# Kernel optimization log

Measured on AMD Instinct MI355X. Metric: run time of the kernel, lower is better.

## Reference

```python
import jax, jax.numpy as jnp
import numpy as np

NUM_HEADS = 16
HEAD_DIM = 128
EMBED_DIM = 2048
BASE = 10000.0


def rope(x, offset=0):
    # x: [b, h, n, d]  rotary positional embedding (lrpe_type=1)
    d = x.shape[-1]
    n = x.shape[-2]
    inv_freq = 1.0 / (BASE ** (jnp.arange(0, d, 2, dtype=jnp.float32) / d))  # [d/2]
    pos = jnp.arange(n, dtype=jnp.float32) + offset                          # [n]
    ang = pos[:, None] * inv_freq[None, :]                                   # [n, d/2]
    cos, sin = jnp.cos(ang), jnp.sin(ang)
    x1, x2 = x[..., 0::2], x[..., 1::2]
    out1 = x1 * cos - x2 * sin
    out2 = x1 * sin + x2 * cos
    return jnp.stack([out1, out2], axis=-1).reshape(x.shape)


def setup_inputs() -> dict:
    key = jax.random.key(0)
    ks = jax.random.split(key, 5)
    b, n = 2, 2048
    std = 0.02
    x = jax.random.normal(ks[0], (b, n, EMBED_DIM), dtype=jnp.float32)
    Wq = jax.random.normal(ks[1], (NUM_HEADS * HEAD_DIM, EMBED_DIM), dtype=jnp.float32) * std
    Wkv = jax.random.normal(ks[2], (2 * HEAD_DIM, EMBED_DIM), dtype=jnp.float32) * std
    Wkvh = jax.random.normal(ks[3], (2 * NUM_HEADS, EMBED_DIM), dtype=jnp.float32) * std
    Wo = jax.random.normal(ks[4], (EMBED_DIM, NUM_HEADS * HEAD_DIM), dtype=jnp.float32) * std
    return {"x": x, "Wq": Wq, "Wkv": Wkv, "Wkvh": Wkvh, "Wo": Wo}


def reference(x, Wq, Wkv, Wkvh, Wo):
    b, n, _ = x.shape
    h, d = NUM_HEADS, HEAD_DIM
    q = x @ Wq.T                     # [b, n, h*d]
    kv = x @ Wkv.T                   # [b, n, 2d]
    kvh = x @ Wkvh.T                 # [b, n, 2h]  (mpa_activation='none')
    k, v = kv[..., :d], kv[..., d:]
    k_head, v_head = kvh[..., :h], kvh[..., h:]
    # gate_type=0: per-token outer product broadcast of the single kv to all heads
    k = jnp.einsum('bnd,bnh->bhnd', k, k_head)
    v = jnp.einsum('bnd,bnh->bhnd', v, v_head)
    q = q.reshape(b, n, h, d).transpose(0, 2, 1, 3)  # [b, h, n, d]
    q = rope(q)
    k = rope(k)
    scale = 1.0 / jnp.sqrt(jnp.float32(d))
    scores = jnp.einsum('bhqd,bhkd->bhqk', q, k) * scale
    causal = jnp.tril(jnp.ones((n, n), dtype=bool))
    scores = jnp.where(causal, scores, -jnp.inf)
    attn = jax.nn.softmax(scores, axis=-1)
    o = jnp.einsum('bhqk,bhkd->bhqd', attn, v)
    o = o.transpose(0, 2, 1, 3).reshape(b, n, h * d)
    return o @ Wo.T
```

## Files before the change

### kernel.cpp

```cpp
#include <hip/hip_runtime.h>
#include <stdint.h>

#define BB 2
#define HH 16
#define NN 2048
#define DD 128
#define EE 2048

typedef short s16x8 __attribute__((ext_vector_type(8)));
typedef float fx4 __attribute__((ext_vector_type(4)));

static __device__ __forceinline__ unsigned short f2bf(float f) {
  unsigned u = __builtin_bit_cast(unsigned, f);
  u += 0x7fffu + ((u >> 16) & 1u);
  return (unsigned short)(u >> 16);
}
static __device__ __forceinline__ float bf2f(unsigned short h) {
  unsigned u = ((unsigned)h) << 16;
  return __builtin_bit_cast(float, u);
}
static __device__ __forceinline__ void gload_lds16(const void* g, void* l) {
  __builtin_amdgcn_global_load_lds(
      (const __attribute__((address_space(1))) unsigned int*)g,
      (__attribute__((address_space(3))) unsigned int*)l, 16, 0, 0);
}
static __device__ __forceinline__ unsigned cvt_pk_bf16(float lo, float hi) {
  unsigned w;
  asm("v_cvt_pk_bf16_f32 %0, %1, %2" : "=v"(w) : "v"(lo), "v"(hi));
  return w;
}

__global__ __launch_bounds__(256) void f2b_all(const float* __restrict__ x,
                                               const float* __restrict__ Wq,
                                               const float* __restrict__ Wkv,
                                               const float* __restrict__ Wo,
                                               const float* __restrict__ Wkvh,
                                               unsigned short* __restrict__ xb,
                                               unsigned short* __restrict__ wqkv,
                                               unsigned short* __restrict__ wob,
                                               unsigned short* __restrict__ wkvhb) {
  int bid = blockIdx.x;
  const float* in;
  unsigned short* out;
  int i;
  if (bid < 8192) { in = x; out = xb; i = bid * 256 + threadIdx.x; }
  else if (bid < 12288) { in = Wq; out = wqkv; i = (bid - 8192) * 256 + threadIdx.x; }
  else if (bid < 12800) { in = Wkv; out = wqkv + 4194304; i = (bid - 12288) * 256 + threadIdx.x; }
  else if (bid < 16896) { in = Wo; out = wob; i = (bid - 12800) * 256 + threadIdx.x; }
  else { in = Wkvh; out = wkvhb; i = (bid - 16896) * 256 + threadIdx.x; }
  float4 v = ((const float4*)in)[i];
  uint2 o;
  o.x = ((unsigned)f2bf(v.y) << 16) | f2bf(v.x);
  o.y = ((unsigned)f2bf(v.w) << 16) | f2bf(v.z);
  ((uint2*)out)[i] = o;
}

#define GBK 64

#define GEMM_STAGE(LDSB, SRCBASE, rowb)                                        \
  _Pragma("unroll") for (int t = 0; t < 4; ++t) {                              \
    int r = wave * 32 + t * 8 + (lane >> 3);                                   \
    int ch = (lane & 7) ^ (r & 7);                                             \
    const unsigned char* src = (SRCBASE) + (size_t)r * (rowb) + ch * 16;       \
    gload_lds16(src, (void*)((LDSB) + (wave * 32 + t * 8) * 128));             \
  }

#define GEMM_LOOP_BODY                                                         \
  for (int k0 = 0; k0 < K; k0 += GBK) {                                        \
    const unsigned char* ag = Ag + (size_t)k0 * 2;                             \
    const unsigned char* bg = Bg + (size_t)k0 * 2;                             \
    __syncthreads();                                                           \
    GEMM_STAGE(Alds, ag, rowb)                                                 \
    GEMM_STAGE(Blds, bg, rowb)                                                 \
    __syncthreads();                                                           \
    _Pragma("unroll") for (int kk = 0; kk < 2; ++kk) {                         \
      s16x8 af[4], bf[4];                                                      \
      _Pragma("unroll") for (int i = 0; i < 4; ++i) {                          \
        int row = wr * 64 + i * 16 + lr;                                       \
        int chunk = (kk * 4 + g) ^ (row & 7);                                  \
        af[i] = *(const s16x8*)(Alds + row * 128 + chunk * 16);                \
      }                                                                        \
      _Pragma("unroll") for (int j = 0; j < 4; ++j) {                          \
        int row = wc * 64 + j * 16 + lr;                                       \
        int chunk = (kk * 4 + g) ^ (row & 7);                                  \
        bf[j] = *(const s16x8*)(Blds + row * 128 + chunk * 16);                \
      }                                                                        \
      _Pragma("unroll") for (int i = 0; i < 4; ++i)                            \
        _Pragma("unroll") for (int j = 0; j < 4; ++j)                          \
          acc[i][j] = __builtin_amdgcn_mfma_f32_16x16x32_bf16(af[i], bf[j],    \
                                                              acc[i][j], 0, 0, 0); \
    }                                                                          \
  }

#define GEMM_PROLOG                                                            \
  __shared__ alignas(16) unsigned char Alds[128 * 128];                        \
  __shared__ alignas(16) unsigned char Blds[128 * 128];                        \
  const int tid = threadIdx.x;                                                 \
  const int wave = tid >> 6, lane = tid & 63;                                  \
  const int g = lane >> 4, lr = lane & 15;                                     \
  const int mtiles = M / 128;                                                  \
  const int mt = blockIdx.x % mtiles, nt = blockIdx.x / mtiles;                \
  const int m0 = mt * 128, n0 = nt * 128;                                      \
  const int wr = wave >> 1, wc = wave & 1;                                     \
  fx4 acc[4][4];                                                               \
  _Pragma("unroll") for (int i = 0; i < 4; ++i)                                \
    _Pragma("unroll") for (int j = 0; j < 4; ++j)                              \
      acc[i][j] = (fx4){0.f, 0.f, 0.f, 0.f};                                   \
  const unsigned char* Ag = (const unsigned char*)(A + (size_t)m0 * K);        \
  const unsigned char* Bg = (const unsigned char*)(B + (size_t)n0 * K);        \
  const size_t rowb = (size_t)K * 2;

__global__ __launch_bounds__(256) void gemm_out(const unsigned short* __restrict__ A,
                                                const unsigned short* __restrict__ B,
                                                float* __restrict__ Cf,
                                                int M, int N, int K) {
  GEMM_PROLOG
  GEMM_LOOP_BODY
#pragma unroll
  for (int i = 0; i < 4; ++i) {
    int row = m0 + wr * 64 + i * 16 + 4 * g;
#pragma unroll
    for (int j = 0; j < 4; ++j) {
      int col = n0 + wc * 64 + j * 16 + lr;
#pragma unroll
      for (int r = 0; r < 4; ++r)
        Cf[(size_t)(row + r) * N + col] = acc[i][j][r];
    }
  }
}

__global__ __launch_bounds__(256) void gemm_qkv(const unsigned short* __restrict__ A,
                                                const unsigned short* __restrict__ B,
                                                unsigned short* __restrict__ qrope,
                                                unsigned short* __restrict__ kvb,
                                                int M, int N, int K) {
  GEMM_PROLOG
  GEMM_LOOP_BODY
#pragma unroll
  for (int j = 0; j < 4; ++j) {
    int col = n0 + wc * 64 + j * 16 + lr;
    if (col < 2048) {
      int hh = col >> 7, d = col & 127;
      float invf = __expf(-0.14391156831212787f * (float)(d >> 1));
      int par = d & 1;
#pragma unroll
      for (int i = 0; i < 4; ++i) {
#pragma unroll
        for (int r = 0; r < 4; ++r) {
          int row = m0 + wr * 64 + i * 16 + 4 * g + r;
          int n = row & (NN - 1), bq = row >> 11;
          float self = acc[i][j][r];
          float other = __shfl_xor(self, 1);
          float sn, cs;
          __sincosf((float)n * invf, &sn, &cs);
          float a = self * cs, bt = other * sn;
          float o = par ? (a + bt) : (a - bt);
          qrope[((size_t)(bq * HH + hh) * NN + n) * DD + d] = f2bf(o);
        }
      }
    } else {
      int c2 = col - 2048;
#pragma unroll
      for (int i = 0; i < 4; ++i) {
#pragma unroll
        for (int r = 0; r < 4; ++r) {
          int row = m0 + wr * 64 + i * 16 + 4 * g + r;
          kvb[(size_t)row * 256 + c2] = f2bf(acc[i][j][r]);
        }
      }
    }
  }
}

__global__ __launch_bounds__(256) void kvh_mfma(const unsigned short* __restrict__ X,
                                                const unsigned short* __restrict__ Wb,
                                                float* __restrict__ out) {
  const int tid = threadIdx.x;
  const int wave = tid >> 6, lane = tid & 63;
  const int g = lane >> 4, lr = lane & 15;
  const int rowbase = blockIdx.x * 32 + (wave & 1) * 16;
  const int colbase = (wave >> 1) * 16;

  const unsigned short* xr = X + (size_t)(rowbase + lr) * EE + 8 * g;
  const unsigned short* wr = Wb + (size_t)(colbase + lr) * EE + 8 * g;

  fx4 acc = (fx4){0.f, 0.f, 0.f, 0.f};
#pragma unroll 8
  for (int k0 = 0; k0 < EE; k0 += 32) {
    s16x8 a = *(const s16x8*)(xr + k0);
    s16x8 b = *(const s16x8*)(wr + k0);
    acc = __builtin_amdgcn_mfma_f32_16x16x32_bf16(a, b, acc, 0, 0, 0);
  }
  const int j = colbase + lr;
  const int head = j & 15, sel = j >> 4;
#pragma unroll
  for (int r = 0; r < 4; ++r) {
    int m = rowbase + 4 * g + r;
    int b = m >> 11, n = m & (NN - 1);
    out[(((size_t)(b * HH + head)) * NN + n) * 2 + sel] = acc[r];
  }
}

__global__ __launch_bounds__(256) void rope_k(const unsigned short* __restrict__ kv,
                                              unsigned short* __restrict__ ko) {
  int idx = blockIdx.x * 256 + threadIdx.x;
  int i = idx & 63;
  int bn = idx >> 6;
  int n = bn & (NN - 1);
  unsigned v = *(const unsigned*)(kv + (size_t)bn * 256 + 2 * i);
  float x1 = bf2f((unsigned short)(v & 0xffff));
  float x2 = bf2f((unsigned short)(v >> 16));
  float inv = __expf(-0.14391156831212787f * (float)i);
  float ang = (float)n * inv;
  float sn, cs;
  __sincosf(ang, &sn, &cs);
  float o1 = x1 * cs - x2 * sn, o2 = x1 * sn + x2 * cs;
  unsigned ov = ((unsigned)f2bf(o2) << 16) | f2bf(o1);
  *(unsigned*)(ko + (size_t)bn * DD + 2 * i) = ov;
}

__global__ __launch_bounds__(256) void vtrans(const unsigned short* __restrict__ kv,
                                              unsigned short* __restrict__ vT) {
  __shared__ unsigned short t[64][40];
  int bx = blockIdx.x;
  int b = bx >> 7;
  int d0 = ((bx >> 5) & 3) * 32;
  int n0 = (bx & 31) * 64;
  int tid = threadIdx.x;
  {
    int i = tid >> 2;
    int c = (tid & 3) * 8;
    s16x8 v = *(const s16x8*)(kv + ((size_t)(b * NN + n0 + i)) * 256 + 128 + d0 + c);
#pragma unroll
    for (int u = 0; u < 8; ++u) t[i][c + u] = (unsigned short)v[u];
  }
  __syncthreads();
  {
    int j = tid >> 3;
    int cc = (tid & 7) * 8;
    s16x8 o;
#pragma unroll
    for (int u = 0; u < 8; ++u) o[u] = (short)t[cc + u][j];
    *(s16x8*)(vT + ((size_t)(b * DD + d0 + j)) * NN + n0 + cc) = o;
  }
}

#define QB 128
#define KB 64

__global__ __launch_bounds__(512, 2) void attn(const unsigned short* __restrict__ Q,
                                               const unsigned short* __restrict__ Kr,
                                               const unsigned short* __restrict__ VT,
                                               const float* __restrict__ KVHP,
                                               unsigned short* __restrict__ O) {
  __shared__ alignas(16) unsigned char Klds[2 * 64 * 256];
  __shared__ alignas(16) unsigned char Vlds[2 * 128 * 128];
  __shared__ alignas(16) unsigned char Plds[16 * 16 * 128];
  __shared__ float2 mlbuf[4][2][16];

  const int qp = blockIdx.x;
  const int h = blockIdx.y;
  const int b = blockIdx.z;
  const int tid = threadIdx.x;
  const int wave = tid >> 6, lane = tid & 63;
  const int parity = wave >> 2, wq = wave & 3;
  const int g = lane >> 4, lr = lane & 15;
  const size_t bh = (size_t)(b * HH + h);

  const float scale2 = 0.08838834764831845f * 1.4426950408889634f;
  const unsigned short* Kb = Kr + (size_t)b * NN * DD;
  const unsigned short* VTb = VT + (size_t)b * DD * NN;
  const float2* KVp = (const float2*)KVHP + (size_t)(b * HH + h) * NN;

  unsigned char* Kl = Klds + parity * (64 * 256);
  unsigned char* Vl = Vlds + parity * (128 * 128);
  float* Obuf = (float*)Plds;

  auto STAGE = [&](int key0s) {
#pragma unroll
    for (int j = 0; j < 4; ++j) {
      int rl = wq * 16 + j * 4 + (lane >> 4);
      int ch = (lane & 15) ^ (rl & 7);
      const unsigned char* gp = (const unsigned char*)(Kb + (size_t)(key0s + rl) * DD) + ch * 16;
      gload_lds16(gp, (void*)(Kl + (wq * 16 + j * 4) * 256));
    }
#pragma unroll
    for (int j = 0; j < 4; ++j) {
      int row = wq * 32 + j * 8 + (lane >> 3);
      int c = lane & 7;
      const unsigned short* gp = VTb + (size_t)row * NN + key0s + ((c ^ (row & 7)) * 8);
      gload_lds16(gp, (void*)(Vl + (wq * 32 + j * 8) * 128));
    }
  };

  auto PHASE = [&](int qt) {
    const int qbase_w = qt * QB + wq * 32;

    s16x8 qf[2][4];
#pragma unroll
    for (int qq = 0; qq < 2; ++qq) {
      const unsigned short* qptr = Q + (bh * NN + qbase_w + qq * 16 + lr) * DD + 8 * g;
#pragma unroll
      for (int dc = 0; dc < 4; ++dc) qf[qq][dc] = *(const s16x8*)(qptr + dc * 32);
    }

    float m_run[2] = {-1e30f, -1e30f}, l_run[2] = {0.f, 0.f};
    fx4 oacc[2][8];
#pragma unroll
    for (int qq = 0; qq < 2; ++qq)
#pragma unroll
      for (int d = 0; d < 8; ++d) oacc[qq][d] = (fx4){0.f, 0.f, 0.f, 0.f};

    const int cnt = qt + 1;
    for (int i = 0; i < cnt; ++i) {
      const int key0 = (2 * i + parity) * KB;
      __syncthreads();
      fx4 khv[4], vhv[4];
#pragma unroll
      for (int kb = 0; kb < 4; ++kb) {
        const float4* kp = (const float4*)(KVp + key0 + kb * 16 + 4 * g);
        float4 f0 = kp[0];
        float4 f1 = kp[1];
        khv[kb] = (fx4){f0.x * scale2, f0.z * scale2, f1.x * scale2, f1.z * scale2};
        vhv[kb] = (fx4){f0.y, f0.w, f1.y, f1.w};
      }
      STAGE(key0);
      __syncthreads();

      if (key0 <= qbase_w + 31) {
        fx4 sacc[2][4];
#pragma unroll
        for (int qq = 0; qq < 2; ++qq)
#pragma unroll
          for (int kb = 0; kb < 4; ++kb) sacc[qq][kb] = (fx4){0.f, 0.f, 0.f, 0.f};
        __builtin_amdgcn_s_setprio(1);
#pragma unroll
        for (int kb = 0; kb < 4; ++kb) {
#pragma unroll
          for (int dc = 0; dc < 4; ++dc) {
            int key = kb * 16 + lr;
            int chunk = (dc * 4 + g) ^ (key & 7);
            s16x8 kf = *(const s16x8*)(Kl + key * 256 + chunk * 16);
            sacc[0][kb] = __builtin_amdgcn_mfma_f32_16x16x32_bf16(kf, qf[0][dc], sacc[0][kb], 0, 0, 0);
            sacc[1][kb] = __builtin_amdgcn_mfma_f32_16x16x32_bf16(kf, qf[1][dc], sacc[1][kb], 0, 0, 0);
          }
        }
        __builtin_amdgcn_s_setprio(0);

#pragma unroll
        for (int qq = 0; qq < 2; ++qq) {
          const int qg = qbase_w + qq * 16 + lr;
          float smax = -1e30f;
          if (key0 + 63 > qbase_w + qq * 16) {
#pragma unroll
            for (int kb = 0; kb < 4; ++kb) {
#pragma unroll
              for (int r = 0; r < 4; ++r) {
                int keyg = key0 + kb * 16 + 4 * g + r;
                float s = sacc[qq][kb][r] * khv[kb][r];
                if (keyg > qg) s = -1e30f;
                sacc[qq][kb][r] = s;
                smax = fmaxf(smax, s);
              }
            }
          } else {
#pragma unroll
            for (int kb = 0; kb < 4; ++kb) {
#pragma unroll
              for (int r = 0; r < 4; ++r) {
                float s = sacc[qq][kb][r] * khv[kb][r];
                sacc[qq][kb][r] = s;
                smax = fmaxf(smax, s);
              }
            }
          }
          smax = fmaxf(smax, __shfl_xor(smax, 16));
          smax = fmaxf(smax, __shfl_xor(smax, 32));
          if (!__all(smax - m_run[qq] <= 8.0f)) {
            float mnew = fmaxf(m_run[qq], smax);
            float corr = exp2f(m_run[qq] - mnew);
            m_run[qq] = mnew;
            l_run[qq] *= corr;
            float cr[4];
#pragma unroll
            for (int r = 0; r < 4; ++r) cr[r] = __shfl(corr, 4 * g + r);
#pragma unroll
            for (int d = 0; d < 8; ++d)
#pragma unroll
              for (int r = 0; r < 4; ++r) oacc[qq][d][r] *= cr[r];
          }
          float rsum = 0.f;
#pragma unroll
          for (int kb = 0; kb < 4; ++kb) {
            float p0 = exp2f(sacc[qq][kb][0] - m_run[qq]);
            float p1 = exp2f(sacc[qq][kb][1] - m_run[qq]);
            float p2 = exp2f(sacc[qq][kb][2] - m_run[qq]);
            float p3 = exp2f(sacc[qq][kb][3] - m_run[qq]);
            rsum += (p0 + p1) + (p2 + p3);
            uint2 w;
            w.x = cvt_pk_bf16(p0 * vhv[kb][0], p1 * vhv[kb][1]);
            w.y = cvt_pk_bf16(p2 * vhv[kb][2], p3 * vhv[kb][3]);
            int chunk = (kb * 2 + (g >> 1)) ^ (lr & 7);
            *(uint2*)(Plds + (wave * 2 + qq) * 2048 + lr * 128 + chunk * 16 + (g & 1) * 8) = w;
          }
          rsum += __shfl_xor(rsum, 16);
          rsum += __shfl_xor(rsum, 32);
          l_run[qq] += rsum;
        }

        s16x8 pa[2][2];
#pragma unroll
        for (int qq = 0; qq < 2; ++qq)
#pragma unroll
          for (int kk = 0; kk < 2; ++kk) {
            int chunk = (kk * 4 + g) ^ (lr & 7);
            pa[qq][kk] = *(const s16x8*)(Plds + (wave * 2 + qq) * 2048 + lr * 128 + chunk * 16);
          }
        __builtin_amdgcn_s_setprio(1);
#pragma unroll
        for (int dc = 0; dc < 8; ++dc) {
#pragma unroll
          for (int kk = 0; kk < 2; ++kk) {
            int d = dc * 16 + lr;
            int chunk = (kk * 4 + g) ^ (d & 7);
            s16x8 vf = *(const s16x8*)(Vl + d * 128 + chunk * 16);
            oacc[0][dc] = __builtin_amdgcn_mfma_f32_16x16x32_bf16(pa[0][kk], vf, oacc[0][dc], 0, 0, 0);
            oacc[1][dc] = __builtin_amdgcn_mfma_f32_16x16x32_bf16(pa[1][kk], vf, oacc[1][dc], 0, 0, 0);
          }
        }
        __builtin_amdgcn_s_setprio(0);
      }
    }

    __syncthreads();
    if (parity == 1 && g == 0) {
#pragma unroll
      for (int qq = 0; qq < 2; ++qq)
        mlbuf[wq][qq][lr] = make_float2(m_run[qq], l_run[qq]);
    }
    __syncthreads();
    float lC[2], af0[2][4], af1[2][4];
    if (parity == 0) {
#pragma unroll
      for (int qq = 0; qq < 2; ++qq) {
        float2 ml1 = mlbuf[wq][qq][lr];
        float M = fmaxf(m_run[qq], ml1.x);
        float a0 = exp2f(m_run[qq] - M);
        float a1 = exp2f(ml1.x - M);
        lC[qq] = l_run[qq] * a0 + ml1.y * a1;
#pragma unroll
        for (int r = 0; r < 4; ++r) {
          af0[qq][r] = __shfl(a0, 4 * g + r);
          af1[qq][r] = __shfl(a1, 4 * g + r);
        }
      }
    }
#pragma unroll
    for (int dh = 0; dh < 2; ++dh) {
      if (parity == 1) {
#pragma unroll
        for (int qq = 0; qq < 2; ++qq)
#pragma unroll
          for (int dc2 = 0; dc2 < 4; ++dc2)
#pragma unroll
            for (int r = 0; r < 4; ++r)
              Obuf[wq * 2048 + (qq * 16 + 4 * g + r) * 64 + dc2 * 16 + lr] =
                  oacc[qq][dh * 4 + dc2][r];
      }
      __syncthreads();
      if (parity == 0) {
#pragma unroll
        for (int qq = 0; qq < 2; ++qq)
#pragma unroll
          for (int dc2 = 0; dc2 < 4; ++dc2)
#pragma unroll
            for (int r = 0; r < 4; ++r) {
              float o1 = Obuf[wq * 2048 + (qq * 16 + 4 * g + r) * 64 + dc2 * 16 + lr];
              oacc[qq][dh * 4 + dc2][r] =
                  oacc[qq][dh * 4 + dc2][r] * af0[qq][r] + o1 * af1[qq][r];
            }
      }
      __syncthreads();
    }
    if (parity == 0) {
#pragma unroll
      for (int qq = 0; qq < 2; ++qq) {
        float inv = 1.0f / lC[qq];
#pragma unroll
        for (int r = 0; r < 4; ++r) {
          float invr = __shfl(inv, 4 * g + r);
          int qout = qbase_w + qq * 16 + 4 * g + r;
          unsigned short* orow = O + (((size_t)b * NN + qout) * HH + h) * DD;
#pragma unroll
          for (int dc = 0; dc < 8; ++dc) orow[dc * 16 + lr] = f2bf(oacc[qq][dc][r] * invr);
        }
      }
    }
  };

  PHASE(qp);
  PHASE(15 - qp);
}

extern "C" void kernel_launch(void* const* d_in, const int* in_sizes, int n_in,
                              void* d_out, int out_size, void* d_ws, size_t ws_size,
                              hipStream_t stream) {
  const float* x = (const float*)d_in[0];
  const float* Wq = (const float*)d_in[1];
  const float* Wkv = (const float*)d_in[2];
  const float* Wkvh = (const float*)d_in[3];
  const float* Wo = (const float*)d_in[4];
  float* out = (float*)d_out;
  char* ws = (char*)d_ws;

  unsigned short* xb    = (unsigned short*)(ws + 0);
  unsigned short* obuf  = xb;
  unsigned short* wqkv  = (unsigned short*)(ws + 16777216);
  unsigned short* wob   = (unsigned short*)(ws + 26214400);
  unsigned short* kvb   = (unsigned short*)(ws + 34603008);
  unsigned short* vtb   = (unsigned short*)(ws + 36700160);
  unsigned short* wkvhb = (unsigned short*)(ws + 53477376);
  float*          kvhb  = (float*)(ws + 53608448);
  unsigned short* qrope = (unsigned short*)(ws + 54132736);
  unsigned short* krope = (unsigned short*)(ws + 70909952);

  f2b_all<<<16960, 256, 0, stream>>>(x, Wq, Wkv, Wo, Wkvh, xb, wqkv, wob, wkvhb);

  gemm_qkv<<<576, 256, 0, stream>>>(xb, wqkv, qrope, kvb, 4096, 2304, 2048);
  kvh_mfma<<<128, 256, 0, stream>>>(xb, wkvhb, kvhb);

  rope_k<<<1024, 256, 0, stream>>>(kvb, krope);
  vtrans<<<256, 256, 0, stream>>>(kvb, vtb);

  dim3 ag(8, HH, BB);
  attn<<<ag, 512, 0, stream>>>(qrope, krope, vtb, kvhb, obuf);

  gemm_out<<<512, 256, 0, stream>>>(obuf, wob, out, 4096, 2048, 2048);
}
```

Before: 214.5 us.

## Read K and V fragments directly from global memory instead of LDS staging

Removes the shared-memory staging of K and V tiles and the two block-wide barriers per key tile. Each wave now loads its MFMA operand fragments straight from global memory, relying on cache hits because K and V are shared across heads. Waves whose key tile is fully masked can skip the iteration early. In exchange, the cross-wave reuse of K and V through LDS is lost and global load latency is exposed on the MFMA critical path, with no explicit prefetch.

```diff
diff --git a/kernel.cpp b/kernel.cpp
--- a/kernel.cpp
+++ b/kernel.cpp
@@ -253,8 +253,6 @@
                                                const unsigned short* __restrict__ VT,
                                                const float* __restrict__ KVHP,
                                                unsigned short* __restrict__ O) {
-  __shared__ alignas(16) unsigned char Klds[2 * 64 * 256];
-  __shared__ alignas(16) unsigned char Vlds[2 * 128 * 128];
   __shared__ alignas(16) unsigned char Plds[16 * 16 * 128];
   __shared__ float2 mlbuf[4][2][16];
 
@@ -272,26 +270,7 @@
   const unsigned short* VTb = VT + (size_t)b * DD * NN;
   const float2* KVp = (const float2*)KVHP + (size_t)(b * HH + h) * NN;
 
-  unsigned char* Kl = Klds + parity * (64 * 256);
-  unsigned char* Vl = Vlds + parity * (128 * 128);
   float* Obuf = (float*)Plds;
-
-  auto STAGE = [&](int key0s) {
-#pragma unroll
-    for (int j = 0; j < 4; ++j) {
-      int rl = wq * 16 + j * 4 + (lane >> 4);
-      int ch = (lane & 15) ^ (rl & 7);
-      const unsigned char* gp = (const unsigned char*)(Kb + (size_t)(key0s + rl) * DD) + ch * 16;
-      gload_lds16(gp, (void*)(Kl + (wq * 16 + j * 4) * 256));
-    }
-#pragma unroll
-    for (int j = 0; j < 4; ++j) {
-      int row = wq * 32 + j * 8 + (lane >> 3);
-      int c = lane & 7;
-      const unsigned short* gp = VTb + (size_t)row * NN + key0s + ((c ^ (row & 7)) * 8);
-      gload_lds16(gp, (void*)(Vl + (wq * 32 + j * 8) * 128));
-    }
-  };
 
   auto PHASE = [&](int qt) {
     const int qbase_w = qt * QB + wq * 32;
@@ -314,7 +293,8 @@
     const int cnt = qt + 1;
     for (int i = 0; i < cnt; ++i) {
       const int key0 = (2 * i + parity) * KB;
-      __syncthreads();
+      if (key0 > qbase_w + 31) continue;
+
       fx4 khv[4], vhv[4];
 #pragma unroll
       for (int kb = 0; kb < 4; ++kb) {
@@ -324,112 +304,106 @@
         khv[kb] = (fx4){f0.x * scale2, f0.z * scale2, f1.x * scale2, f1.z * scale2};
         vhv[kb] = (fx4){f0.y, f0.w, f1.y, f1.w};
       }
-      STAGE(key0);
-      __syncthreads();
-
-      if (key0 <= qbase_w + 31) {
-        fx4 sacc[2][4];
-#pragma unroll
-        for (int qq = 0; qq < 2; ++qq)
-#pragma unroll
-          for (int kb = 0; kb < 4; ++kb) sacc[qq][kb] = (fx4){0.f, 0.f, 0.f, 0.f};
-        __builtin_amdgcn_s_setprio(1);
-#pragma unroll
-        for (int kb = 0; kb < 4; ++kb) {
-#pragma unroll
-          for (int dc = 0; dc < 4; ++dc) {
-            int key = kb * 16 + lr;
-            int chunk = (dc * 4 + g) ^ (key & 7);
-            s16x8 kf = *(const s16x8*)(Kl + key * 256 + chunk * 16);
-            sacc[0][kb] = __builtin_amdgcn_mfma_f32_16x16x32_bf16(kf, qf[0][dc], sacc[0][kb], 0, 0, 0);
-            sacc[1][kb] = __builtin_amdgcn_mfma_f32_16x16x32_bf16(kf, qf[1][dc], sacc[1][kb], 0, 0, 0);
-          }
-        }
-        __builtin_amdgcn_s_setprio(0);
-
-#pragma unroll
-        for (int qq = 0; qq < 2; ++qq) {
-          const int qg = qbase_w + qq * 16 + lr;
-          float smax = -1e30f;
-          if (key0 + 63 > qbase_w + qq * 16) {
-#pragma unroll
-            for (int kb = 0; kb < 4; ++kb) {
-#pragma unroll
-              for (int r = 0; r < 4; ++r) {
-                int keyg = key0 + kb * 16 + 4 * g + r;
-                float s = sacc[qq][kb][r] * khv[kb][r];
-                if (keyg > qg) s = -1e30f;
-                sacc[qq][kb][r] = s;
-                smax = fmaxf(smax, s);
-              }
-            }
-          } else {
-#pragma unroll
-            for (int kb = 0; kb < 4; ++kb) {
-#pragma unroll
-              for (int r = 0; r < 4; ++r) {
-                float s = sacc[qq][kb][r] * khv[kb][r];
-                sacc[qq][kb][r] = s;
-                smax = fmaxf(smax, s);
-              }
+
+      fx4 sacc[2][4];
+#pragma unroll
+      for (int qq = 0; qq < 2; ++qq)
+#pragma unroll
+        for (int kb = 0; kb < 4; ++kb) sacc[qq][kb] = (fx4){0.f, 0.f, 0.f, 0.f};
+      __builtin_amdgcn_s_setprio(1);
+#pragma unroll
+      for (int kb = 0; kb < 4; ++kb) {
+        const unsigned short* krow = Kb + (size_t)(key0 + kb * 16 + lr) * DD + 8 * g;
+#pragma unroll
+        for (int dc = 0; dc < 4; ++dc) {
+          s16x8 kf = *(const s16x8*)(krow + dc * 32);
+          sacc[0][kb] = __builtin_amdgcn_mfma_f32_16x16x32_bf16(kf, qf[0][dc], sacc[0][kb], 0, 0, 0);
+          sacc[1][kb] = __builtin_amdgcn_mfma_f32_16x16x32_bf16(kf, qf[1][dc], sacc[1][kb], 0, 0, 0);
+        }
+      }
+      __builtin_amdgcn_s_setprio(0);
+
+#pragma unroll
+      for (int qq = 0; qq < 2; ++qq) {
+        const int qg = qbase_w + qq * 16 + lr;
+        float smax = -1e30f;
+        if (key0 + 63 > qbase_w + qq * 16) {
+#pragma unroll
+          for (int kb = 0; kb < 4; ++kb) {
+#pragma unroll
+            for (int r = 0; r < 4; ++r) {
+              int keyg = key0 + kb * 16 + 4 * g + r;
+              float s = sacc[qq][kb][r] * khv[kb][r];
+              if (keyg > qg) s = -1e30f;
+              sacc[qq][kb][r] = s;
+              smax = fmaxf(smax, s);
             }
           }
-          smax = fmaxf(smax, __shfl_xor(smax, 16));
-          smax = fmaxf(smax, __shfl_xor(smax, 32));
-          if (!__all(smax - m_run[qq] <= 8.0f)) {
-            float mnew = fmaxf(m_run[qq], smax);
-            float corr = exp2f(m_run[qq] - mnew);
-            m_run[qq] = mnew;
-            l_run[qq] *= corr;
-            float cr[4];
-#pragma unroll
-            for (int r = 0; r < 4; ++r) cr[r] = __shfl(corr, 4 * g + r);
-#pragma unroll
-            for (int d = 0; d < 8; ++d)
-#pragma unroll
-              for (int r = 0; r < 4; ++r) oacc[qq][d][r] *= cr[r];
+        } else {
+#pragma unroll
+          for (int kb = 0; kb < 4; ++kb) {
+#pragma unroll
+            for (int r = 0; r < 4; ++r) {
+              float s = sacc[qq][kb][r] * khv[kb][r];
+              sacc[qq][kb][r] = s;
+              smax = fmaxf(smax, s);
+            }
           }
-          float rsum = 0.f;
-#pragma unroll
-          for (int kb = 0; kb < 4; ++kb) {
-            float p0 = exp2f(sacc[qq][kb][0] - m_run[qq]);
-            float p1 = exp2f(sacc[qq][kb][1] - m_run[qq]);
-            float p2 = exp2f(sacc[qq][kb][2] - m_run[qq]);
-            float p3 = exp2f(sacc[qq][kb][3] - m_run[qq]);
-            rsum += (p0 + p1) + (p2 + p3);
-            uint2 w;
-            w.x = cvt_pk_bf16(p0 * vhv[kb][0], p1 * vhv[kb][1]);
-            w.y = cvt_pk_bf16(p2 * vhv[kb][2], p3 * vhv[kb][3]);
-            int chunk = (kb * 2 + (g >> 1)) ^ (lr & 7);
-            *(uint2*)(Plds + (wave * 2 + qq) * 2048 + lr * 128 + chunk * 16 + (g & 1) * 8) = w;
-          }
-          rsum += __shfl_xor(rsum, 16);
-          rsum += __shfl_xor(rsum, 32);
-          l_run[qq] += rsum;
-        }
-
-        s16x8 pa[2][2];
-#pragma unroll
-        for (int qq = 0; qq < 2; ++qq)
-#pragma unroll
-          for (int kk = 0; kk < 2; ++kk) {
-            int chunk = (kk * 4 + g) ^ (lr & 7);
-            pa[qq][kk] = *(const s16x8*)(Plds + (wave * 2 + qq) * 2048 + lr * 128 + chunk * 16);
-          }
-        __builtin_amdgcn_s_setprio(1);
-#pragma unroll
-        for (int dc = 0; dc < 8; ++dc) {
-#pragma unroll
-          for (int kk = 0; kk < 2; ++kk) {
-            int d = dc * 16 + lr;
-            int chunk = (kk * 4 + g) ^ (d & 7);
-            s16x8 vf = *(const s16x8*)(Vl + d * 128 + chunk * 16);
-            oacc[0][dc] = __builtin_amdgcn_mfma_f32_16x16x32_bf16(pa[0][kk], vf, oacc[0][dc], 0, 0, 0);
-            oacc[1][dc] = __builtin_amdgcn_mfma_f32_16x16x32_bf16(pa[1][kk], vf, oacc[1][dc], 0, 0, 0);
-          }
-        }
-        __builtin_amdgcn_s_setprio(0);
-      }
+        }
+        smax = fmaxf(smax, __shfl_xor(smax, 16));
+        smax = fmaxf(smax, __shfl_xor(smax, 32));
+        if (!__all(smax - m_run[qq] <= 8.0f)) {
+          float mnew = fmaxf(m_run[qq], smax);
+          float corr = exp2f(m_run[qq] - mnew);
+          m_run[qq] = mnew;
+          l_run[qq] *= corr;
+          float cr[4];
+#pragma unroll
+          for (int r = 0; r < 4; ++r) cr[r] = __shfl(corr, 4 * g + r);
+#pragma unroll
+          for (int d = 0; d < 8; ++d)
+#pragma unroll
+            for (int r = 0; r < 4; ++r) oacc[qq][d][r] *= cr[r];
+        }
+        float rsum = 0.f;
+#pragma unroll
+        for (int kb = 0; kb < 4; ++kb) {
+          float p0 = exp2f(sacc[qq][kb][0] - m_run[qq]);
+          float p1 = exp2f(sacc[qq][kb][1] - m_run[qq]);
+          float p2 = exp2f(sacc[qq][kb][2] - m_run[qq]);
+          float p3 = exp2f(sacc[qq][kb][3] - m_run[qq]);
+          rsum += (p0 + p1) + (p2 + p3);
+          uint2 w;
+          w.x = cvt_pk_bf16(p0 * vhv[kb][0], p1 * vhv[kb][1]);
+          w.y = cvt_pk_bf16(p2 * vhv[kb][2], p3 * vhv[kb][3]);
+          int chunk = (kb * 2 + (g >> 1)) ^ (lr & 7);
+          *(uint2*)(Plds + (wave * 2 + qq) * 2048 + lr * 128 + chunk * 16 + (g & 1) * 8) = w;
+        }
+        rsum += __shfl_xor(rsum, 16);
+        rsum += __shfl_xor(rsum, 32);
+        l_run[qq] += rsum;
+      }
+
+      s16x8 pa[2][2];
+#pragma unroll
+      for (int qq = 0; qq < 2; ++qq)
+#pragma unroll
+        for (int kk = 0; kk < 2; ++kk) {
+          int chunk = (kk * 4 + g) ^ (lr & 7);
+          pa[qq][kk] = *(const s16x8*)(Plds + (wave * 2 + qq) * 2048 + lr * 128 + chunk * 16);
+        }
+      __builtin_amdgcn_s_setprio(1);
+#pragma unroll
+      for (int dc = 0; dc < 8; ++dc) {
+        const unsigned short* vrow = VTb + (size_t)(dc * 16 + lr) * NN + key0 + 8 * g;
+#pragma unroll
+        for (int kk = 0; kk < 2; ++kk) {
+          s16x8 vf = *(const s16x8*)(vrow + kk * 32);
+          oacc[0][dc] = __builtin_amdgcn_mfma_f32_16x16x32_bf16(pa[0][kk], vf, oacc[0][dc], 0, 0, 0);
+          oacc[1][dc] = __builtin_amdgcn_mfma_f32_16x16x32_bf16(pa[1][kk], vf, oacc[1][dc], 0, 0, 0);
+        }
+      }
+      __builtin_amdgcn_s_setprio(0);
     }
 
     __syncthreads();
```

Measured after the change: 268.9 us. 25.4% more time.
